# Kernel tuning notes

Measured on AMD Instinct MI355X. Metric: run time of the kernel, lower is better.

Reference implementation:

```python
import jax, jax.numpy as jnp
import numpy as np

HIDDEN = 32  # hard-coded in the module


def _lstm_cell(x, h, c, W_ih, W_hh, b_ih, b_hh):
    # torch.nn.LSTMCell: gates in order i, f, g, o
    gates = x @ W_ih.T + b_ih + h @ W_hh.T + b_hh
    i, f, g, o = jnp.split(gates, 4, axis=-1)
    c_new = jax.nn.sigmoid(f) * c + jax.nn.sigmoid(i) * jnp.tanh(g)
    h_new = jax.nn.sigmoid(o) * jnp.tanh(c_new)
    return h_new, c_new


def setup_inputs() -> dict:
    key = jax.random.key(0)
    ks = jax.random.split(key, 11)
    B, T, d, len_out = 256, 1024, 8, 10
    s = 0.05
    return {
        "input": jax.random.normal(ks[0], (B, T, d), dtype=jnp.float32),
        "W_ih1": jax.random.normal(ks[1], (4 * HIDDEN, d), dtype=jnp.float32) * s,
        "W_hh1": jax.random.normal(ks[2], (4 * HIDDEN, HIDDEN), dtype=jnp.float32) * s,
        "b_ih1": jax.random.normal(ks[3], (4 * HIDDEN,), dtype=jnp.float32) * s,
        "b_hh1": jax.random.normal(ks[4], (4 * HIDDEN,), dtype=jnp.float32) * s,
        "W_ih2": jax.random.normal(ks[5], (4 * HIDDEN, HIDDEN), dtype=jnp.float32) * s,
        "W_hh2": jax.random.normal(ks[6], (4 * HIDDEN, HIDDEN), dtype=jnp.float32) * s,
        "b_ih2": jax.random.normal(ks[7], (4 * HIDDEN,), dtype=jnp.float32) * s,
        "b_hh2": jax.random.normal(ks[8], (4 * HIDDEN,), dtype=jnp.float32) * s,
        "W_lin": jax.random.normal(ks[9], (d * len_out, HIDDEN), dtype=jnp.float32) * s,
        "b_lin": jax.random.normal(ks[10], (d * len_out,), dtype=jnp.float32) * s,
    }


def reference(input, W_ih1, W_hh1, b_ih1, b_hh1, W_ih2, W_hh2, b_ih2, b_hh2, W_lin, b_lin):
    B, T, d = input.shape
    len_out = W_lin.shape[0] // d

    def step(carry, x_t):
        h1, c1, h2, c2 = carry
        h1, c1 = _lstm_cell(x_t, h1, c1, W_ih1, W_hh1, b_ih1, b_hh1)
        h2, c2 = _lstm_cell(h1, h2, c2, W_ih2, W_hh2, b_ih2, b_hh2)
        out = h2 @ W_lin.T + b_lin  # [B, d*len_out]
        return (h1, c1, h2, c2), out

    z = jnp.zeros((B, HIDDEN), dtype=input.dtype)
    init = (z, z, z, z)
    xs = jnp.swapaxes(input, 0, 1)  # [T, B, d]
    _, outs = jax.lax.scan(step, init, xs)  # [T, B, d*len_out]
    outs = jnp.swapaxes(outs, 0, 1)  # [B, T, d*len_out]
    return outs.reshape(B, T, d, len_out)
```

## Files before the change

kernel.cpp:

```cpp
#include <hip/hip_runtime.h>

#define TT  1024
#define DIN 8

__device__ __forceinline__ float fsig(float x) {
    float e = __builtin_amdgcn_exp2f(-1.4426950408889634f * x);
    return __builtin_amdgcn_rcpf(1.0f + e);
}
__device__ __forceinline__ float ftanh_(float x) {
    float e = __builtin_amdgcn_exp2f(-2.8853900817779268f * x);
    return 2.0f * __builtin_amdgcn_rcpf(1.0f + e) - 1.0f;
}
template<int CTRL>
__device__ __forceinline__ float dppf(float v) {
    return __uint_as_float((unsigned)__builtin_amdgcn_update_dpp(
        0, (int)__float_as_uint(v), CTRL, 0xF, 0xF, true));
}

__global__ void __launch_bounds__(512, 2)
lstm_pipe8(const float* __restrict__ x,
           const float* __restrict__ Wih1, const float* __restrict__ Whh1,
           const float* __restrict__ bih1, const float* __restrict__ bhh1,
           const float* __restrict__ Wih2, const float* __restrict__ Whh2,
           const float* __restrict__ bih2, const float* __restrict__ bhh2,
           const float* __restrict__ Wlin, const float* __restrict__ blin,
           float* __restrict__ out)
{
    const int tid  = threadIdx.x;
    const int wv   = tid >> 6;
    const int l    = tid & 63;
    const int part = l & 1;
    const int g    = (l >> 1) & 3;
    const int ul   = l >> 3;
    const int b    = blockIdx.x;
    const bool isL1 = (wv < 4);
    const int  wu   = isL1 ? wv : (wv - 4);
    const int  unit = wu*8 + ul;
    const int  R    = g*32 + unit;
    const bool isg  = (g == 2);

    __shared__ float hb1[2][32];
    __shared__ float hb2[2][32];
    if (tid < 64)       ((float*)hb1)[tid]      = 0.f;
    else if (tid < 128) ((float*)hb2)[tid - 64] = 0.f;

    float wg[20];
    float wg2[32];
    float wl[16];
    float bias = 0.f, obias = 0.f;
    int ocol = 0;

    if (isL1) {
        const float* wsrc = Whh1 + R*32 + part*16;
#pragma unroll
        for (int qq = 0; qq < 4; ++qq) {
            float4 v = reinterpret_cast<const float4*>(wsrc)[qq];
            wg[4*qq]=v.x; wg[4*qq+1]=v.y; wg[4*qq+2]=v.z; wg[4*qq+3]=v.w;
        }
        float4 xv = *reinterpret_cast<const float4*>(Wih1 + R*DIN + part*4);
        wg[16]=xv.x; wg[17]=xv.y; wg[18]=xv.z; wg[19]=xv.w;
        if (!part) bias = bih1[R] + bhh1[R];
        ocol = wu*20 + (l >> 1);
        const int oc = (l < 40) ? ocol : 79;
        const float* osrc = Wlin + oc*32 + part*16;
#pragma unroll
        for (int qq = 0; qq < 4; ++qq) {
            float4 v = reinterpret_cast<const float4*>(osrc)[qq];
            wl[4*qq]=v.x; wl[4*qq+1]=v.y; wl[4*qq+2]=v.z; wl[4*qq+3]=v.w;
        }
        if (!part) obias = blin[oc];
    } else {
        const float* wsrc = part ? (Wih2 + R*32) : (Whh2 + R*32);
#pragma unroll
        for (int qq = 0; qq < 8; ++qq) {
            float4 v = reinterpret_cast<const float4*>(wsrc)[qq];
            wg2[4*qq]=v.x; wg2[4*qq+1]=v.y; wg2[4*qq+2]=v.z; wg2[4*qq+3]=v.w;
        }
        if (!part) bias = bih2[R] + bhh2[R];
    }

    float c = 0.f;

    const float* __restrict__ xb = x   + (size_t)b * (TT*DIN);
    float* __restrict__ outb     = out + (size_t)b * (TT*80);

    float4 xcur;
    if (isL1) xcur = *reinterpret_cast<const float4*>(xb + part*4);

    __syncthreads();

#pragma unroll 1
    for (int t = 0; t <= TT + 1; ++t) {
        const int pm1 = (t - 1) & 1;
        const int p0  = t & 1;

        if (isL1) {
            if (t < TT) {
                const float* hin = &hb1[pm1][part << 4];
                float a0 = bias, a1 = 0.f, a2 = 0.f, a3 = 0.f;
#pragma unroll
                for (int qq = 0; qq < 4; ++qq) {
                    float4 v = reinterpret_cast<const float4*>(hin)[qq];
                    a0 += wg[4*qq]  *v.x; a1 += wg[4*qq+1]*v.y;
                    a2 += wg[4*qq+2]*v.z; a3 += wg[4*qq+3]*v.w;
                }
                a0 += wg[16]*xcur.x; a1 += wg[17]*xcur.y;
                a2 += wg[18]*xcur.z; a3 += wg[19]*xcur.w;
                const int tn = (t + 1 < TT) ? (t + 1) : (TT - 1);
                xcur = *reinterpret_cast<const float4*>(xb + tn*DIN + part*4);

                float sum  = (a0 + a1) + (a2 + a3);
                float full = sum + dppf<0xB1>(sum);
                float u  = isg ? (full + full) : full;
                float S  = fsig(u);
                float av = isg ? (S + S - 1.0f) : S;
                float itg = dppf<0x114>(av) * av;
                float fv  = dppf<0x112>(av);
                c = fv * c + itg;
                float so  = dppf<0x102>(av);
                float hv  = so * ftanh_(c);
                if ((l & 7) == 4) hb1[p0][unit] = hv;
            }
            if (t >= 2) {
                const float* hob = &hb2[p0][part << 4];
                float o0 = obias, o1 = 0.f, o2 = 0.f, o3 = 0.f;
#pragma unroll
                for (int qq = 0; qq < 4; ++qq) {
                    float4 v = reinterpret_cast<const float4*>(hob)[qq];
                    o0 += wl[4*qq]  *v.x; o1 += wl[4*qq+1]*v.y;
                    o2 += wl[4*qq+2]*v.z; o3 += wl[4*qq+3]*v.w;
                }
                float osum  = (o0 + o1) + (o2 + o3);
                float ofull = osum + dppf<0xB1>(osum);
                if (!part && l < 40)
                    outb[(size_t)(t - 2)*80 + ocol] = ofull;
            }
        } else {
            if (t >= 1 && t <= TT) {
                const float* hin = part ? &hb1[pm1][0] : &hb2[p0][0];
                float a0 = bias, a1 = 0.f, a2 = 0.f, a3 = 0.f;
#pragma unroll
                for (int qq = 0; qq < 8; ++qq) {
                    float4 v = reinterpret_cast<const float4*>(hin)[qq];
                    a0 += wg2[4*qq]  *v.x; a1 += wg2[4*qq+1]*v.y;
                    a2 += wg2[4*qq+2]*v.z; a3 += wg2[4*qq+3]*v.w;
                }
                float sum  = (a0 + a1) + (a2 + a3);
                float full = sum + dppf<0xB1>(sum);
                float u  = isg ? (full + full) : full;
                float S  = fsig(u);
                float av = isg ? (S + S - 1.0f) : S;
                float itg = dppf<0x114>(av) * av;
                float fv  = dppf<0x112>(av);
                c = fv * c + itg;
                float so  = dppf<0x102>(av);
                float hv  = so * ftanh_(c);
                if ((l & 7) == 4) hb2[pm1][unit] = hv;
            }
        }

        __syncthreads();
    }
}

extern "C" void kernel_launch(void* const* d_in, const int* in_sizes, int n_in,
                              void* d_out, int out_size, void* d_ws, size_t ws_size,
                              hipStream_t stream) {
    const float* x    = (const float*)d_in[0];
    const float* Wih1 = (const float*)d_in[1];
    const float* Whh1 = (const float*)d_in[2];
    const float* bih1 = (const float*)d_in[3];
    const float* bhh1 = (const float*)d_in[4];
    const float* Wih2 = (const float*)d_in[5];
    const float* Whh2 = (const float*)d_in[6];
    const float* bih2 = (const float*)d_in[7];
    const float* bhh2 = (const float*)d_in[8];
    const float* Wlin = (const float*)d_in[9];
    const float* blin = (const float*)d_in[10];

    const int B = in_sizes[0] / (TT * DIN);

    hipLaunchKernelGGL(lstm_pipe8, dim3(B), dim3(512), 0, stream,
                       x, Wih1, Whh1, bih1, bhh1,
                       Wih2, Whh2, bih2, bhh2, Wlin, blin,
                       (float*)d_out);
}
```

Before: 442.2 us.

## Move output projection to a separate batched kernel and rebalance layer-2 matvec

The recurrent kernel no longer computes the final linear projection inside the time loop. It writes the layer-2 hidden state into the output buffer, and a second kernel then applies W_lin over all timesteps in tiles, reading and overwriting that buffer in place. Layer-2 work is also redistributed: each lane now holds two 16-wide weight slices, and partial sums are exchanged across lanes with a DPP row rotate. This shortens the serial per-step critical path and drops one loop iteration, at the cost of an extra kernel launch and an extra global round-trip of the hidden states.

```diff
diff --git a/kernel.cpp b/kernel.cpp
--- a/kernel.cpp
+++ b/kernel.cpp
@@ -18,13 +18,12 @@
 }
 
 __global__ void __launch_bounds__(512, 2)
-lstm_pipe8(const float* __restrict__ x,
-           const float* __restrict__ Wih1, const float* __restrict__ Whh1,
-           const float* __restrict__ bih1, const float* __restrict__ bhh1,
-           const float* __restrict__ Wih2, const float* __restrict__ Whh2,
-           const float* __restrict__ bih2, const float* __restrict__ bhh2,
-           const float* __restrict__ Wlin, const float* __restrict__ blin,
-           float* __restrict__ out)
+lstm_rec(const float* __restrict__ x,
+         const float* __restrict__ Wih1, const float* __restrict__ Whh1,
+         const float* __restrict__ bih1, const float* __restrict__ bhh1,
+         const float* __restrict__ Wih2, const float* __restrict__ Whh2,
+         const float* __restrict__ bih2, const float* __restrict__ bhh2,
+         float* __restrict__ out)
 {
     const int tid  = threadIdx.x;
     const int wv   = tid >> 6;
@@ -36,7 +35,6 @@
     const bool isL1 = (wv < 4);
     const int  wu   = isL1 ? wv : (wv - 4);
     const int  unit = wu*8 + ul;
-    const int  R    = g*32 + unit;
     const bool isg  = (g == 2);
 
     __shared__ float hb1[2][32];
@@ -45,12 +43,11 @@
     else if (tid < 128) ((float*)hb2)[tid - 64] = 0.f;
 
     float wg[20];
-    float wg2[32];
-    float wl[16];
-    float bias = 0.f, obias = 0.f;
-    int ocol = 0;
+    float wA[16], wB[16];
+    float bias = 0.f;
 
     if (isL1) {
+        const int R = g*32 + unit;
         const float* wsrc = Whh1 + R*32 + part*16;
 #pragma unroll
         for (int qq = 0; qq < 4; ++qq) {
@@ -60,23 +57,21 @@
         float4 xv = *reinterpret_cast<const float4*>(Wih1 + R*DIN + part*4);
         wg[16]=xv.x; wg[17]=xv.y; wg[18]=xv.z; wg[19]=xv.w;
         if (!part) bias = bih1[R] + bhh1[R];
-        ocol = wu*20 + (l >> 1);
-        const int oc = (l < 40) ? ocol : 79;
-        const float* osrc = Wlin + oc*32 + part*16;
+    } else {
+        const int hs = g & 1;
+        const int k2 = g >> 1;
+        const int Re = (2*k2)*32 + unit;
+        const int Ro = (2*k2+1)*32 + unit;
+        const int Rw = g*32 + unit;
+        const float* base = part ? Wih2 : Whh2;
 #pragma unroll
         for (int qq = 0; qq < 4; ++qq) {
-            float4 v = reinterpret_cast<const float4*>(osrc)[qq];
-            wl[4*qq]=v.x; wl[4*qq+1]=v.y; wl[4*qq+2]=v.z; wl[4*qq+3]=v.w;
-        }
-        if (!part) obias = blin[oc];
-    } else {
-        const float* wsrc = part ? (Wih2 + R*32) : (Whh2 + R*32);
-#pragma unroll
-        for (int qq = 0; qq < 8; ++qq) {
-            float4 v = reinterpret_cast<const float4*>(wsrc)[qq];
-            wg2[4*qq]=v.x; wg2[4*qq+1]=v.y; wg2[4*qq+2]=v.z; wg2[4*qq+3]=v.w;
-        }
-        if (!part) bias = bih2[R] + bhh2[R];
+            float4 va = reinterpret_cast<const float4*>(base + Re*32 + hs*16)[qq];
+            wA[4*qq]=va.x; wA[4*qq+1]=va.y; wA[4*qq+2]=va.z; wA[4*qq+3]=va.w;
+            float4 vb = reinterpret_cast<const float4*>(base + Ro*32 + hs*16)[qq];
+            wB[4*qq]=vb.x; wB[4*qq+1]=vb.y; wB[4*qq+2]=vb.z; wB[4*qq+3]=vb.w;
+        }
+        bias = bih2[Rw] + bhh2[Rw];
     }
 
     float c = 0.f;
@@ -86,13 +81,15 @@
 
     float4 xcur;
     if (isL1) xcur = *reinterpret_cast<const float4*>(xb + part*4);
+    int xoff = DIN;
+    int o2   = 0;
 
     __syncthreads();
 
 #pragma unroll 1
-    for (int t = 0; t <= TT + 1; ++t) {
-        const int pm1 = (t - 1) & 1;
+    for (int t = 0; t <= TT; ++t) {
         const int p0  = t & 1;
+        const int pm1 = p0 ^ 1;
 
         if (isL1) {
             if (t < TT) {
@@ -106,8 +103,8 @@
                 }
                 a0 += wg[16]*xcur.x; a1 += wg[17]*xcur.y;
                 a2 += wg[18]*xcur.z; a3 += wg[19]*xcur.w;
-                const int tn = (t + 1 < TT) ? (t + 1) : (TT - 1);
-                xcur = *reinterpret_cast<const float4*>(xb + tn*DIN + part*4);
+                xcur = *reinterpret_cast<const float4*>(xb + xoff + part*4);
+                xoff = (xoff + DIN > (TT-1)*DIN) ? (TT-1)*DIN : (xoff + DIN);
 
                 float sum  = (a0 + a1) + (a2 + a3);
                 float full = sum + dppf<0xB1>(sum);
@@ -121,32 +118,31 @@
                 float hv  = so * ftanh_(c);
                 if ((l & 7) == 4) hb1[p0][unit] = hv;
             }
-            if (t >= 2) {
-                const float* hob = &hb2[p0][part << 4];
-                float o0 = obias, o1 = 0.f, o2 = 0.f, o3 = 0.f;
+        } else {
+            if (t >= 1) {
+                const int hs = g & 1;
+                const float* hin = part ? &hb1[pm1][hs << 4] : &hb2[p0][hs << 4];
+                float4 hv4[4];
+#pragma unroll
+                for (int qq = 0; qq < 4; ++qq)
+                    hv4[qq] = reinterpret_cast<const float4*>(hin)[qq];
+                float e0 = 0.f, e1 = 0.f, o0 = 0.f, o1 = 0.f;
 #pragma unroll
                 for (int qq = 0; qq < 4; ++qq) {
-                    float4 v = reinterpret_cast<const float4*>(hob)[qq];
-                    o0 += wl[4*qq]  *v.x; o1 += wl[4*qq+1]*v.y;
-                    o2 += wl[4*qq+2]*v.z; o3 += wl[4*qq+3]*v.w;
+                    e0 += wA[4*qq]  *hv4[qq].x; e1 += wA[4*qq+1]*hv4[qq].y;
+                    e0 += wA[4*qq+2]*hv4[qq].z; e1 += wA[4*qq+3]*hv4[qq].w;
+                    o0 += wB[4*qq]  *hv4[qq].x; o1 += wB[4*qq+1]*hv4[qq].y;
+                    o0 += wB[4*qq+2]*hv4[qq].z; o1 += wB[4*qq+3]*hv4[qq].w;
                 }
-                float osum  = (o0 + o1) + (o2 + o3);
-                float ofull = osum + dppf<0xB1>(osum);
-                if (!part && l < 40)
-                    outb[(size_t)(t - 2)*80 + ocol] = ofull;
-            }
-        } else {
-            if (t >= 1 && t <= TT) {
-                const float* hin = part ? &hb1[pm1][0] : &hb2[p0][0];
-                float a0 = bias, a1 = 0.f, a2 = 0.f, a3 = 0.f;
-#pragma unroll
-                for (int qq = 0; qq < 8; ++qq) {
-                    float4 v = reinterpret_cast<const float4*>(hin)[qq];
-                    a0 += wg2[4*qq]  *v.x; a1 += wg2[4*qq+1]*v.y;
-                    a2 += wg2[4*qq+2]*v.z; a3 += wg2[4*qq+3]*v.w;
-                }
-                float sum  = (a0 + a1) + (a2 + a3);
-                float full = sum + dppf<0xB1>(sum);
+                float accE = e0 + e1;
+                float accO = o0 + o1;
+                accE += dppf<0xB1>(accE);
+                accO += dppf<0xB1>(accO);
+                float stage = hs ? accE : accO;
+                float recv  = dppf<0x4E>(stage);
+                float own   = hs ? accO : accE;
+                float full  = own + recv + bias;
+
                 float u  = isg ? (full + full) : full;
                 float S  = fsig(u);
                 float av = isg ? (S + S - 1.0f) : S;
@@ -155,11 +151,71 @@
                 c = fv * c + itg;
                 float so  = dppf<0x102>(av);
                 float hv  = so * ftanh_(c);
-                if ((l & 7) == 4) hb2[pm1][unit] = hv;
+                if ((l & 7) == 4) {
+                    hb2[pm1][unit] = hv;
+                    outb[o2 + unit] = hv;
+                }
+                o2 += 80;
             }
         }
 
         __syncthreads();
+    }
+}
+
+__global__ void __launch_bounds__(256, 4)
+out_lin(const float* __restrict__ Wlin, const float* __restrict__ blin,
+        float* __restrict__ out, int ntiles)
+{
+    __shared__ float wl[80][36];
+    __shared__ float bl[80];
+    __shared__ float ht[16][36];
+    const int tid = threadIdx.x;
+
+#pragma unroll 1
+    for (int i = tid; i < 640; i += 256) {
+        const int cc = i >> 3, qq = i & 7;
+        float4 v = reinterpret_cast<const float4*>(Wlin)[i];
+        *reinterpret_cast<float4*>(&wl[cc][qq*4]) = v;
+    }
+    if (tid < 80) bl[tid] = blin[tid];
+    __syncthreads();
+
+    const int row = tid >> 4;
+    const int cl  = tid & 15;
+
+#pragma unroll 1
+    for (int tile = blockIdx.x; tile < ntiles; tile += gridDim.x) {
+        const size_t base = (size_t)tile * 16;
+        if (tid < 128) {
+            const int r = tid >> 3, qq = tid & 7;
+            float4 v = *reinterpret_cast<const float4*>(out + (base + r)*80 + qq*4);
+            *reinterpret_cast<float4*>(&ht[r][qq*4]) = v;
+        }
+        __syncthreads();
+
+        float hr[32];
+#pragma unroll
+        for (int j = 0; j < 8; ++j) {
+            float4 v = *reinterpret_cast<const float4*>(&ht[row][j*4]);
+            hr[4*j]=v.x; hr[4*j+1]=v.y; hr[4*j+2]=v.z; hr[4*j+3]=v.w;
+        }
+        float res[5];
+#pragma unroll
+        for (int cj = 0; cj < 5; ++cj) {
+            const int cc = cl + 16*cj;
+            float a0 = bl[cc], a1 = 0.f, a2 = 0.f, a3 = 0.f;
+#pragma unroll
+            for (int k = 0; k < 32; k += 4) {
+                a0 += wl[cc][k]  *hr[k];   a1 += wl[cc][k+1]*hr[k+1];
+                a2 += wl[cc][k+2]*hr[k+2]; a3 += wl[cc][k+3]*hr[k+3];
+            }
+            res[cj] = (a0 + a1) + (a2 + a3);
+        }
+        __syncthreads();
+#pragma unroll
+        for (int cj = 0; cj < 5; ++cj)
+            out[(base + row)*80 + cl + 16*cj] = res[cj];
     }
 }
 
@@ -179,9 +235,12 @@
     const float* blin = (const float*)d_in[10];
 
     const int B = in_sizes[0] / (TT * DIN);
-
-    hipLaunchKernelGGL(lstm_pipe8, dim3(B), dim3(512), 0, stream,
+    const int ntiles = (B * TT) / 16;
+
+    hipLaunchKernelGGL(lstm_rec, dim3(B), dim3(512), 0, stream,
                        x, Wih1, Whh1, bih1, bhh1,
-                       Wih2, Whh2, bih2, bhh2, Wlin, blin,
+                       Wih2, Whh2, bih2, bhh2,
                        (float*)d_out);
-}
+    hipLaunchKernelGGL(out_lin, dim3(2048), dim3(256), 0, stream,
+                       Wlin, blin, (float*)d_out, ntiles);
+}
```

New measurement: 392.7 us. 11.2% less time.
